# Optimization experiments

Hardware: AMD Instinct MI355X
Metric: run time of the kernel (lower is better)

The kernel has to match this reference:

```python
import jax, jax.numpy as jnp
import numpy as np

B, L, D = 2, 1024, 1024
H, KV, CH = 16, 4, 8          # attn heads, kv heads, context-manager heads
HD = D // H                   # 64
E, K, FF = 8, 2, 4 * D        # experts, top-k, ffn hidden
DC = 4                        # conv kernel size
EPS = 1e-6


def setup_inputs() -> dict:
    key = jax.random.key(0)
    ks = jax.random.split(key, 32)
    s = 0.02
    n = lambda k, shp: jax.random.normal(k, shp, jnp.float32) * s
    return {
        'x': jax.random.normal(ks[0], (B, L, D), jnp.float32),
        'mask': jnp.ones((B, L), jnp.int32),
        'w_rms1': jnp.ones((D,), jnp.float32),
        'w_rms2': jnp.ones((D,), jnp.float32),
        'w_rms3': jnp.ones((D,), jnp.float32),
        'w_rms4': jnp.ones((D,), jnp.float32),
        'Wq': n(ks[1], (D, D)), 'Wk': n(ks[2], (D, KV * HD)),
        'Wv': n(ks[3], (D, KV * HD)), 'Wo': n(ks[4], (D, D)),
        'Cq': n(ks[5], (D, D)), 'Ck': n(ks[6], (D, D)),
        'Cv': n(ks[7], (D, D)), 'Co': n(ks[8], (D, D)),
        'Wi': n(ks[9], (D, 2 * D)), 'bi': jnp.zeros((2 * D,), jnp.float32),
        'conv_w': n(ks[10], (D, 1, DC)), 'conv_b': jnp.zeros((D,), jnp.float32),
        'Wod': n(ks[11], (D, D)), 'bod': jnp.zeros((D,), jnp.float32),
        'w_gate': n(ks[12], (E, D)),
        'W1': n(ks[13], (E, D, FF)), 'b1': jnp.zeros((E, FF), jnp.float32),
        'W2': n(ks[14], (E, FF, D)), 'b2': jnp.zeros((E, D), jnp.float32),
    }


def _rmsnorm(x, w):
    rms = jnp.sqrt(jnp.mean(x * x, axis=-1, keepdims=True) + EPS)
    return w * (x / rms)


def _mha(x, mask, Wq, Wk, Wv, Wo, nh, nkv):
    b, l, d = x.shape
    hd = d // nh
    q = (x @ Wq).reshape(b, l, nh, hd)
    k = (x @ Wk).reshape(b, l, nkv, hd)
    v = (x @ Wv).reshape(b, l, nkv, hd)
    if nh != nkv:
        rep = nh // nkv
        k = jnp.repeat(k, rep, axis=2)
        v = jnp.repeat(v, rep, axis=2)
    scores = jnp.einsum('bqhd,bkhd->bhqk', q, k) * (hd ** -0.5)
    scores = jnp.where(mask[:, None, None, :] == 0, -jnp.inf, scores)
    attn = jax.nn.softmax(scores, axis=-1)
    out = jnp.einsum('bhqk,bkhd->bqhd', attn, v).reshape(b, l, d)
    return out @ Wo


def _deltanet(x, Wi, bi, conv_w, conv_b, Wod, bod):
    gv = x @ Wi + bi
    gate, value = jnp.split(gv, 2, axis=-1)
    # depthwise causal conv1d (kernel DC, left pad DC-1, truncated to L)
    v_ncl = jnp.transpose(value, (0, 2, 1))  # [B, D, L]
    conv = jax.lax.conv_general_dilated(
        v_ncl, conv_w, window_strides=(1,), padding=[(DC - 1, 0)],
        feature_group_count=D, dimension_numbers=('NCH', 'OIH', 'NCH'))
    conv = conv + conv_b[None, :, None]
    conv = jnp.transpose(conv, (0, 2, 1))  # [B, L, D]
    gated = conv * jax.nn.silu(gate)
    return gated @ Wod + bod


def _moe(x, w_gate, W1, b1, W2, b2):
    b, l, d = x.shape
    flat = x.reshape(-1, d)                                  # [T, D]
    gate = jax.nn.softmax(flat @ w_gate.T, axis=-1)          # [T, E]
    topk_scores, topk_idx = jax.lax.top_k(gate, K)           # [T, K]
    onehot = jax.nn.one_hot(topk_idx, E, dtype=flat.dtype)   # [T, K, E]
    combine = jnp.sum(topk_scores[..., None] * onehot, axis=1)  # [T, E]
    h = jnp.einsum('td,edh->teh', flat, W1) + b1
    h = jax.nn.gelu(h, approximate=False)
    y = jnp.einsum('teh,ehd->ted', h, W2) + b2
    out = jnp.einsum('ted,te->td', y, combine)
    return out.reshape(b, l, d)


def reference(x, mask, w_rms1, w_rms2, w_rms3, w_rms4,
              Wq, Wk, Wv, Wo, Cq, Ck, Cv, Co,
              Wi, bi, conv_w, conv_b, Wod, bod,
              w_gate, W1, b1, W2, b2):
    # eval mode: dropout = identity. multi_token_pred output is discarded by the block.
    res1 = x
    h = _rmsnorm(x, w_rms1)
    h = res1 + _mha(h, mask, Wq, Wk, Wv, Wo, H, KV)
    res2 = h
    # ContextManager stand-in: 8-head softmax self-attention (source unavailable)
    cm = _mha(h, mask, Cq, Ck, Cv, Co, CH, CH)
    h = res2 + cm
    res3 = h
    g = _rmsnorm(h, w_rms2)
    h = res3 + _deltanet(g, Wi, bi, conv_w, conv_b, Wod, bod)
    res4 = h
    g = _rmsnorm(h, w_rms3)
    h = res4 + _moe(g, w_gate, W1, b1, W2, b2)
    h = _rmsnorm(h, w_rms4)
    return h
```

## Files before the change

kernel.cpp:

```cpp
#include <hip/hip_runtime.h>
#include <hip/hip_bf16.h>
#include <math.h>

#define T_TOK 2048
#define B_SZ 2
#define L_SEQ 1024
#define D_MOD 1024
#define N_H 16
#define N_KV 4
#define N_CH 8
#define N_E 8
#define FF_DIM 4096
#define DC_K 4
#define EPS_F 1e-6f

typedef unsigned short u16;
typedef unsigned int u32;
typedef short s16x8 __attribute__((ext_vector_type(8)));
typedef u16 u16x8 __attribute__((ext_vector_type(8)));
typedef float f32x4 __attribute__((ext_vector_type(4)));
struct alignas(8) U16x4 { u16 a, b, c, d; };

__device__ __forceinline__ float gelu_exact(float x) {
    return 0.5f * x * (1.0f + erff(x * 0.70710678118654752f));
}
__device__ __forceinline__ u16 f2bf(float f) {
    u32 x = __float_as_uint(f);
    return (u16)((x + 0x7fffu + ((x >> 16) & 1u)) >> 16);
}
__device__ __forceinline__ float b2f(u16 u) {
    return __uint_as_float(((u32)u) << 16);
}
__device__ __forceinline__ void gload_lds16(const u16* g, u16* l) {
    __builtin_amdgcn_global_load_lds(
        (const __attribute__((address_space(1))) u32*)g,
        (__attribute__((address_space(3))) u32*)l, 16, 0, 0);
}

struct TDesc {
    const float* src;
    u16* dst;
    int R, C, dstStride, dstRowOff, tileBase, nPerMat;
};
struct TPack { TDesc d[12]; };

__global__ __launch_bounds__(256) void transpose_all(TPack p) {
    __shared__ float ts[64][65];
    int t = blockIdx.x;
    int i = 0;
#pragma unroll
    for (int j = 1; j < 12; ++j)
        if (t >= p.d[j].tileBase) i = j;
    TDesc d = p.d[i];
    int local = t - d.tileBase;
    int e = local / d.nPerMat;
    local -= e * d.nPerMat;
    int ntx = d.C >> 6;
    int bx = local % ntx, by = local / ntx;
    const float* src = d.src + (size_t)e * d.R * d.C;
    u16* dst = d.dst + (size_t)e * (size_t)d.C * d.dstStride;
    int c0 = bx * 64, r0 = by * 64;
    int tid = threadIdx.x;
#pragma unroll
    for (int k = 0; k < 4; ++k) {
        int fidx = k * 256 + tid;
        int r = fidx >> 4, c4 = (fidx & 15) << 2;
        float4 v = *(const float4*)(src + (size_t)(r0 + r) * d.C + c0 + c4);
        ts[r][c4] = v.x; ts[r][c4 + 1] = v.y; ts[r][c4 + 2] = v.z; ts[r][c4 + 3] = v.w;
    }
    __syncthreads();
#pragma unroll
    for (int k = 0; k < 2; ++k) {
        int idx = k * 256 + tid;
        int c = idx >> 3;
        int r8 = (idx & 7) << 3;
        u16x8 o;
#pragma unroll
        for (int j = 0; j < 8; ++j) o[j] = f2bf(ts[r8 + j][c]);
        *(u16x8*)(dst + (size_t)(d.dstRowOff + c0 + c) * d.dstStride + r0 + r8) = o;
    }
}

__global__ __launch_bounds__(256) void rmsnorm_kernel(const float* __restrict__ x,
                                                      const float* __restrict__ w,
                                                      float* __restrict__ fo,
                                                      u16* __restrict__ bo) {
    int row = blockIdx.x;
    int tid = threadIdx.x;
    const float* xr = x + (size_t)row * D_MOD;
    float4 v = ((const float4*)xr)[tid];
    float ss = v.x * v.x + v.y * v.y + v.z * v.z + v.w * v.w;
    __shared__ float red[256];
    red[tid] = ss;
    __syncthreads();
    for (int s = 128; s > 0; s >>= 1) {
        if (tid < s) red[tid] += red[tid + s];
        __syncthreads();
    }
    float inv = 1.0f / sqrtf(red[0] * (1.0f / D_MOD) + EPS_F);
    float4 wv = ((const float4*)w)[tid];
    float4 o;
    o.x = v.x * inv * wv.x;
    o.y = v.y * inv * wv.y;
    o.z = v.z * inv * wv.z;
    o.w = v.w * inv * wv.w;
    if (fo) ((float4*)(fo + (size_t)row * D_MOD))[tid] = o;
    if (bo) {
        U16x4 b;
        b.a = f2bf(o.x); b.b = f2bf(o.y); b.c = f2bf(o.z); b.d = f2bf(o.w);
        *(U16x4*)(bo + (size_t)row * D_MOD + tid * 4) = b;
    }
}

template <int MODE, int GELU, int OUTF, int OUTB, int BM>
__global__ __launch_bounds__(256) void mfma_gemm(const u16* __restrict__ A,
                                                 const u16* __restrict__ BT,
                                                 const float* __restrict__ bias,
                                                 const float* __restrict__ res,
                                                 float* __restrict__ C,
                                                 u16* __restrict__ Cb,
                                                 const int* __restrict__ list,
                                                 const int* __restrict__ offs,
                                                 const int* __restrict__ counts,
                                                 int M, int N, int K, int nx) {
    constexpr int PWR = BM / 2;
    constexpr int MI = PWR / 16;
    constexpr int NI = 4;
    constexpr int NAI = (BM >= 64) ? (BM / 64) : 1;
    __shared__ u16 ldsA[2][BM * 32];
    __shared__ u16 ldsB[2][128 * 32];
    int tid = threadIdx.x;
    int lane = tid & 63, w = tid >> 6;
    int wr = w >> 1, wc = w & 1;
    int bx, by, e;
    if (MODE == 0) {
        bx = blockIdx.x; by = blockIdx.y; e = 0;
    } else {
        int id = blockIdx.x;
        e = id & 7;
        int r = id >> 3;
        bx = r % nx;
        by = r / nx;
    }
    int cnt, off;
    if (MODE == 0) { cnt = M; off = 0; }
    else { cnt = counts[e]; off = offs[e]; }
    int m0 = by * BM;
    if (m0 >= cnt) return;
    int n0 = bx * 128;
    const u16* Bt = BT + (size_t)e * (size_t)N * K;

    const u16* aSrc[NAI];
    const u16* bSrc[2];
#pragma unroll
    for (int j = 0; j < NAI; ++j) {
        int rowA = (BM >= 64) ? (j * 64 + w * 16 + (lane >> 2))
                              : (w * 16 + (lane >> 2));
        int slot = lane & 3;
        int rl = m0 + ((rowA < BM) ? rowA : (BM - 1));
        if (rl >= cnt) rl = cnt - 1;
        size_t ga;
        if (MODE == 1) ga = (size_t)list[off + rl] * K;
        else if (MODE == 2) ga = (size_t)(off + rl) * K;
        else ga = (size_t)rl * K;
        aSrc[j] = A + ga + ((slot ^ ((rowA >> 1) & 3)) << 3);
    }
#pragma unroll
    for (int j = 0; j < 2; ++j) {
        int rowB = j * 64 + w * 16 + (lane >> 2);
        int slot = lane & 3;
        bSrc[j] = Bt + (size_t)(n0 + rowB) * K + ((slot ^ ((rowB >> 1) & 3)) << 3);
    }

    auto stage = [&](int buf, int k0) {
        if constexpr (BM == 32) {
            if (w < 2) gload_lds16(aSrc[0] + k0, &ldsA[buf][w * 512]);
        } else {
#pragma unroll
            for (int j = 0; j < NAI; ++j)
                gload_lds16(aSrc[j] + k0, &ldsA[buf][(j * 256 + w * 64) * 8]);
        }
#pragma unroll
        for (int j = 0; j < 2; ++j)
            gload_lds16(bSrc[j] + k0, &ldsB[buf][(j * 256 + w * 64) * 8]);
    };

    f32x4 acc[MI][NI] = {};
    int r16 = lane & 15, cr = lane >> 4;

    stage(0, 0);
    __syncthreads();
    int cur = 0;
    for (int k0 = 0; k0 < K; k0 += 32) {
        if (k0 + 32 < K) stage(cur ^ 1, k0 + 32);
        s16x8 af[MI], bfr[NI];
#pragma unroll
        for (int mi = 0; mi < MI; ++mi) {
            int row = wr * PWR + mi * 16 + r16;
            af[mi] = *(const s16x8*)&ldsA[cur][row * 32 + ((cr ^ ((row >> 1) & 3)) << 3)];
        }
#pragma unroll
        for (int ni = 0; ni < NI; ++ni) {
            int row = wc * 64 + ni * 16 + r16;
            bfr[ni] = *(const s16x8*)&ldsB[cur][row * 32 + ((cr ^ ((row >> 1) & 3)) << 3)];
        }
#pragma unroll
        for (int mi = 0; mi < MI; ++mi)
#pragma unroll
            for (int ni = 0; ni < NI; ++ni)
                acc[mi][ni] = __builtin_amdgcn_mfma_f32_16x16x32_bf16(af[mi], bfr[ni],
                                                                      acc[mi][ni], 0, 0, 0);
        __syncthreads();
        cur ^= 1;
    }

    const float* bias_e = bias ? (bias + (MODE ? (size_t)e * N : 0)) : nullptr;
#pragma unroll
    for (int mi = 0; mi < MI; ++mi) {
#pragma unroll
        for (int ni = 0; ni < NI; ++ni) {
            int rloc = wr * PWR + mi * 16 + (lane >> 4) * 4;
            int col = n0 + wc * 64 + ni * 16 + (lane & 15);
#pragma unroll
            for (int jj = 0; jj < 4; ++jj) {
                int rl = m0 + rloc + jj;
                if (rl >= cnt) continue;
                float val = acc[mi][ni][jj];
                if (bias_e) val += bias_e[col];
                if (GELU) val = gelu_exact(val);
                size_t crow = (MODE == 0) ? (size_t)rl : (size_t)(off + rl);
                if (res) val += res[crow * N + col];
                if (OUTF) C[crow * N + col] = val;
                if (OUTB) Cb[crow * N + col] = f2bf(val);
            }
        }
    }
}

template <int HD>
__global__ __launch_bounds__(256) void mfma_attn(const u16* __restrict__ Qb,
                                                 const u16* __restrict__ Kb,
                                                 const u16* __restrict__ Vb,
                                                 u16* __restrict__ O,
                                                 int stride, int ostride,
                                                 int nh, int nkv, float scale) {
    constexpr int KT = 64;
    constexpr int CH = HD / 8;
    constexpr int NF = HD / 32;
    constexpr int ND = HD / 16;
    constexpr int VSTR = 72;
    constexpr int NISS = (64 * CH) / (64 * 4);

    __shared__ u16 Kl[64 * HD];
    __shared__ u16 Vt[HD * VSTR];
    __shared__ u16 Pl[4][16 * 72];

    int tid = threadIdx.x, lane = tid & 63, w = tid >> 6;
    int g = lane >> 4, r16 = lane & 15;
    int q0 = blockIdx.x * 64, h = blockIdx.y, b = blockIdx.z;
    int kvh = h / (nh / nkv);

    const u16* Qp = Qb + (size_t)(b * L_SEQ + q0 + w * 16 + r16) * stride + h * HD + g * 8;
    s16x8 qf[NF];
#pragma unroll
    for (int f = 0; f < NF; ++f) qf[f] = *(const s16x8*)(Qp + f * 32);

    const u16* Kbase = Kb + (size_t)(b * L_SEQ) * stride + (size_t)kvh * HD;
    const u16* Vbase = Vb + (size_t)(b * L_SEQ) * stride + (size_t)kvh * HD;

    int srcOffK[NISS];
#pragma unroll
    for (int i = 0; i < NISS; ++i) {
        int ci = (w * NISS + i) * 64 + lane;
        int row = ci / CH;
        int ch = ci % CH;
        srcOffK[i] = row * stride + ((ch ^ (row & 7)) << 3);
    }

    f32x4 ofr[ND] = {};
    float m_r[4], l_r[4];
#pragma unroll
    for (int r = 0; r < 4; ++r) { m_r[r] = -1e30f; l_r[r] = 0.f; }

    for (int kt = 0; kt < L_SEQ / KT; ++kt) {
        const u16* Ksrc = Kbase + (size_t)(kt * KT) * stride;
        const u16* Vsrc = Vbase + (size_t)(kt * KT) * stride;
        __syncthreads();
#pragma unroll
        for (int i = 0; i < NISS; ++i)
            gload_lds16(Ksrc + srcOffK[i], Kl + (size_t)(w * NISS + i) * 512);
#pragma unroll
        for (int half = 0; half < HD / 64; ++half) {
            int dbase = w * 16 + half * 64;
            u16x8 v0 = *(const u16x8*)(Vsrc + (size_t)lane * stride + dbase);
            u16x8 v1 = *(const u16x8*)(Vsrc + (size_t)lane * stride + dbase + 8);
#pragma unroll
            for (int j = 0; j < 8; ++j) {
                Vt[(dbase + j) * VSTR + lane] = v0[j];
                Vt[(dbase + 8 + j) * VSTR + lane] = v1[j];
            }
        }
        __syncthreads();

        f32x4 s[4];
#pragma unroll
        for (int sub = 0; sub < 4; ++sub) {
            f32x4 acc = {};
#pragma unroll
            for (int f = 0; f < NF; ++f) {
                int row = sub * 16 + r16;
                int chunk = (f * 4 + g) ^ (row & 7);
                s16x8 kf = *(const s16x8*)&Kl[(row * CH + chunk) * 8];
                acc = __builtin_amdgcn_mfma_f32_16x16x32_bf16(qf[f], kf, acc, 0, 0, 0);
            }
            s[sub] = acc;
        }

#pragma unroll
        for (int sub = 0; sub < 4; ++sub)
#pragma unroll
            for (int r = 0; r < 4; ++r) s[sub][r] *= scale;
#pragma unroll
        for (int r = 0; r < 4; ++r) {
            float mx = fmaxf(fmaxf(s[0][r], s[1][r]), fmaxf(s[2][r], s[3][r]));
            mx = fmaxf(mx, __shfl_xor(mx, 1));
            mx = fmaxf(mx, __shfl_xor(mx, 2));
            mx = fmaxf(mx, __shfl_xor(mx, 4));
            mx = fmaxf(mx, __shfl_xor(mx, 8));
            float mo = m_r[r];
            float mn = fmaxf(mo, mx);
            float sc = __expf(mo - mn);
            m_r[r] = mn;
            float sum = 0.f;
#pragma unroll
            for (int sub = 0; sub < 4; ++sub) {
                float e = __expf(s[sub][r] - mn);
                s[sub][r] = e;
                sum += e;
            }
            sum += __shfl_xor(sum, 1);
            sum += __shfl_xor(sum, 2);
            sum += __shfl_xor(sum, 4);
            sum += __shfl_xor(sum, 8);
            l_r[r] = l_r[r] * sc + sum;
#pragma unroll
            for (int dsub = 0; dsub < ND; ++dsub) ofr[dsub][r] *= sc;
        }

        u16* Pw = Pl[w];
#pragma unroll
        for (int sub = 0; sub < 4; ++sub)
#pragma unroll
            for (int r = 0; r < 4; ++r) {
                int q = g * 4 + r;
                int k = sub * 16 + r16;
                Pw[q * 72 + (((k >> 3) ^ (q & 7)) << 3) + (k & 7)] = f2bf(s[sub][r]);
            }
        __syncthreads();

        s16x8 pf[2];
#pragma unroll
        for (int ks = 0; ks < 2; ++ks) {
            int chunk = (ks * 4 + g) ^ (r16 & 7);
            pf[ks] = *(const s16x8*)&Pw[r16 * 72 + chunk * 8];
        }
#pragma unroll
        for (int dsub = 0; dsub < ND; ++dsub)
#pragma unroll
            for (int ks = 0; ks < 2; ++ks) {
                s16x8 vf = *(const s16x8*)&Vt[(dsub * 16 + r16) * VSTR + ks * 32 + g * 8];
                ofr[dsub] = __builtin_amdgcn_mfma_f32_16x16x32_bf16(pf[ks], vf, ofr[dsub], 0, 0, 0);
            }
    }

    float inv[4];
#pragma unroll
    for (int r = 0; r < 4; ++r) inv[r] = 1.0f / l_r[r];
#pragma unroll
    for (int dsub = 0; dsub < ND; ++dsub)
#pragma unroll
        for (int r = 0; r < 4; ++r) {
            int q = q0 + w * 16 + g * 4 + r;
            O[(size_t)(b * L_SEQ + q) * ostride + h * HD + dsub * 16 + r16] =
                f2bf(ofr[dsub][r] * inv[r]);
        }
}

__global__ __launch_bounds__(256) void conv_gate_kernel(const u16* __restrict__ gv,
                                                        const float* __restrict__ cw,
                                                        const float* __restrict__ cb,
                                                        u16* __restrict__ gated) {
    int idx = blockIdx.x * 256 + threadIdx.x;
    if (idx >= T_TOK * D_MOD) return;
    int d = idx & (D_MOD - 1);
    int t = idx >> 10;
    int l = t & (L_SEQ - 1);
    float conv = cb[d];
#pragma unroll
    for (int i = 0; i < DC_K; ++i) {
        int lp = l - (DC_K - 1) + i;
        if (lp >= 0)
            conv += b2f(gv[(size_t)(t - l + lp) * (2 * D_MOD) + D_MOD + d]) * cw[d * DC_K + i];
    }
    float gate = b2f(gv[(size_t)t * (2 * D_MOD) + d]);
    float sig = 1.0f / (1.0f + expf(-gate));
    gated[(size_t)t * D_MOD + d] = f2bf(conv * (gate * sig));
}

__global__ __launch_bounds__(256) void route_kernel(const float* __restrict__ g,
                                                    const float* __restrict__ wg,
                                                    int* __restrict__ tIdx,
                                                    float* __restrict__ tScore,
                                                    int* __restrict__ counts) {
    int t = blockIdx.x, tid = threadIdx.x;
    __shared__ float gs[D_MOD];
    __shared__ float logits[N_E];
    ((float4*)gs)[tid] = ((const float4*)(g + (size_t)t * D_MOD))[tid];
    __syncthreads();
    int e = tid >> 5, lane = tid & 31;
    const float* w = wg + (size_t)e * D_MOD;
    float p = 0.f;
    for (int d = lane; d < D_MOD; d += 32) p += gs[d] * w[d];
    for (int o = 16; o > 0; o >>= 1) p += __shfl_down(p, o, 32);
    if (lane == 0) logits[e] = p;
    __syncthreads();
    if (tid == 0) {
        float mx = logits[0];
        for (int e2 = 1; e2 < N_E; ++e2) mx = fmaxf(mx, logits[e2]);
        float pe[N_E];
        float Z = 0.f;
        for (int e2 = 0; e2 < N_E; ++e2) {
            pe[e2] = expf(logits[e2] - mx);
            Z += pe[e2];
        }
        int i0 = 0;
        float b0 = pe[0];
        for (int e2 = 1; e2 < N_E; ++e2)
            if (pe[e2] > b0) { b0 = pe[e2]; i0 = e2; }
        int i1 = -1;
        float b1 = -1.f;
        for (int e2 = 0; e2 < N_E; ++e2)
            if (e2 != i0 && pe[e2] > b1) { b1 = pe[e2]; i1 = e2; }
        float invZ = 1.0f / Z;
        tIdx[t * 2] = i0;
        tIdx[t * 2 + 1] = i1;
        tScore[t * 2] = b0 * invZ;
        tScore[t * 2 + 1] = b1 * invZ;
        atomicAdd(&counts[i0], 1);
        atomicAdd(&counts[i1], 1);
    }
}

__global__ void prefix_kernel(const int* __restrict__ counts, int* __restrict__ offs,
                              int* __restrict__ cursor) {
    if (threadIdx.x == 0) {
        int acc = 0;
        for (int e = 0; e < N_E; ++e) {
            offs[e] = acc;
            acc += counts[e];
            cursor[e] = 0;
        }
    }
}

__global__ __launch_bounds__(256) void fill_kernel(const int* __restrict__ tIdx,
                                                   const int* __restrict__ offs,
                                                   int* __restrict__ cursor,
                                                   int* __restrict__ list,
                                                   int* __restrict__ pairRow) {
    int t = blockIdx.x * 256 + threadIdx.x;
    if (t >= T_TOK) return;
    for (int kk = 0; kk < 2; ++kk) {
        int e = tIdx[t * 2 + kk];
        int pos = atomicAdd(&cursor[e], 1);
        int slot = offs[e] + pos;
        list[slot] = t;
        pairRow[t * 2 + kk] = slot;
    }
}

__global__ __launch_bounds__(256) void combine_rms_kernel(const u16* __restrict__ ysel,
                                                          const float* __restrict__ tScore,
                                                          const int* __restrict__ pairRow,
                                                          const float* __restrict__ h,
                                                          const float* __restrict__ w,
                                                          float* __restrict__ out) {
    int row = blockIdx.x;
    int tid = threadIdx.x;
    float4 v = ((const float4*)(h + (size_t)row * D_MOD))[tid];
    int r0 = pairRow[row * 2], r1 = pairRow[row * 2 + 1];
    float s0 = tScore[row * 2], s1 = tScore[row * 2 + 1];
    U16x4 y0 = *(const U16x4*)(ysel + (size_t)r0 * D_MOD + tid * 4);
    U16x4 y1 = *(const U16x4*)(ysel + (size_t)r1 * D_MOD + tid * 4);
    v.x += s0 * b2f(y0.a) + s1 * b2f(y1.a);
    v.y += s0 * b2f(y0.b) + s1 * b2f(y1.b);
    v.z += s0 * b2f(y0.c) + s1 * b2f(y1.c);
    v.w += s0 * b2f(y0.d) + s1 * b2f(y1.d);
    __shared__ float red[256];
    red[tid] = v.x * v.x + v.y * v.y + v.z * v.z + v.w * v.w;
    __syncthreads();
    for (int s = 128; s > 0; s >>= 1) {
        if (tid < s) red[tid] += red[tid + s];
        __syncthreads();
    }
    float inv = 1.0f / sqrtf(red[0] * (1.0f / D_MOD) + EPS_F);
    float4 wv = ((const float4*)w)[tid];
    float4 o;
    o.x = v.x * inv * wv.x;
    o.y = v.y * inv * wv.y;
    o.z = v.z * inv * wv.z;
    o.w = v.w * inv * wv.w;
    ((float4*)(out + (size_t)row * D_MOD))[tid] = o;
}

extern "C" void kernel_launch(void* const* d_in, const int* in_sizes, int n_in,
                              void* d_out, int out_size, void* d_ws, size_t ws_size,
                              hipStream_t stream) {
    const float* x = (const float*)d_in[0];
    const float* w_rms1 = (const float*)d_in[2];
    const float* w_rms2 = (const float*)d_in[3];
    const float* w_rms3 = (const float*)d_in[4];
    const float* w_rms4 = (const float*)d_in[5];
    const float* Wq = (const float*)d_in[6];
    const float* Wk = (const float*)d_in[7];
    const float* Wv = (const float*)d_in[8];
    const float* Wo = (const float*)d_in[9];
    const float* Cq = (const float*)d_in[10];
    const float* Ck = (const float*)d_in[11];
    const float* Cv = (const float*)d_in[12];
    const float* Co = (const float*)d_in[13];
    const float* Wi = (const float*)d_in[14];
    const float* bi = (const float*)d_in[15];
    const float* conv_w = (const float*)d_in[16];
    const float* conv_b = (const float*)d_in[17];
    const float* Wod = (const float*)d_in[18];
    const float* bod = (const float*)d_in[19];
    const float* w_gate = (const float*)d_in[20];
    const float* W1 = (const float*)d_in[21];
    const float* b1 = (const float*)d_in[22];
    const float* W2 = (const float*)d_in[23];
    const float* b2 = (const float*)d_in[24];
    float* out = (float*)d_out;

    char* ws = (char*)d_ws;
    size_t off = 0;
    auto alloc_f = [&](size_t n) { float* p = (float*)(ws + off); off += n * 4; return p; };
    auto alloc_b = [&](size_t n) { u16* p = (u16*)(ws + off); off += n * 2; return p; };

    u16* qkvT = alloc_b((size_t)1536 * 1024);
    u16* cqkvT = alloc_b((size_t)3072 * 1024);
    u16* WoT = alloc_b((size_t)1024 * 1024);
    u16* CoT = alloc_b((size_t)1024 * 1024);
    u16* WiT = alloc_b((size_t)2048 * 1024);
    u16* WodT = alloc_b((size_t)1024 * 1024);
    u16* W1T = alloc_b((size_t)N_E * FF_DIM * 1024);
    u16* W2T = alloc_b((size_t)N_E * 1024 * FF_DIM);
    const size_t TD = (size_t)T_TOK * D_MOD;
    float* h = alloc_f(TD);
    float* nrm = alloc_f(TD);
    u16* nrm_bf = alloc_b(TD);
    u16* h_bf = alloc_b(TD);
    u16* ab_bf = alloc_b(TD);
    u16* qkv_bf = alloc_b((size_t)T_TOK * 3072);
    u16* gv_bf = alloc_b((size_t)T_TOK * 2048);
    u16* hsel = alloc_b((size_t)2 * T_TOK * FF_DIM);
    u16* ysel = alloc_b((size_t)2 * T_TOK * D_MOD);
    int* counts = (int*)(ws + off); off += N_E * 4;
    int* offs = (int*)(ws + off); off += N_E * 4;
    int* cursor = (int*)(ws + off); off += N_E * 4;
    int* tIdx = (int*)(ws + off); off += 2 * T_TOK * 4;
    int* list = (int*)(ws + off); off += 2 * T_TOK * 4;
    int* pairRow = (int*)(ws + off); off += 2 * T_TOK * 4;
    float* tScore = alloc_f(2 * T_TOK);

    TPack tp;
    int tb = 0;
    auto mkd = [&](int i, const float* s, u16* d, int R, int C, int ds, int ro, int nmat) {
        int per = (C >> 6) * (R >> 6);
        tp.d[i] = TDesc{s, d, R, C, ds, ro, tb, per};
        tb += per * nmat;
    };
    mkd(0, Wq, qkvT, 1024, 1024, 1024, 0, 1);
    mkd(1, Wk, qkvT, 1024, 256, 1024, 1024, 1);
    mkd(2, Wv, qkvT, 1024, 256, 1024, 1280, 1);
    mkd(3, Cq, cqkvT, 1024, 1024, 1024, 0, 1);
    mkd(4, Ck, cqkvT, 1024, 1024, 1024, 1024, 1);
    mkd(5, Cv, cqkvT, 1024, 1024, 1024, 2048, 1);
    mkd(6, Wo, WoT, 1024, 1024, 1024, 0, 1);
    mkd(7, Co, CoT, 1024, 1024, 1024, 0, 1);
    mkd(8, Wi, WiT, 1024, 2048, 1024, 0, 1);
    mkd(9, Wod, WodT, 1024, 1024, 1024, 0, 1);
    mkd(10, W1, W1T, 1024, FF_DIM, 1024, 0, N_E);
    mkd(11, W2, W2T, FF_DIM, 1024, FF_DIM, 0, N_E);
    transpose_all<<<tb, 256, 0, stream>>>(tp);

    rmsnorm_kernel<<<T_TOK, 256, 0, stream>>>(x, w_rms1, nullptr, nrm_bf);
    mfma_gemm<0, 0, 0, 1, 32><<<dim3(12, 64, 1), 256, 0, stream>>>(
        nrm_bf, qkvT, nullptr, nullptr, nullptr, qkv_bf, nullptr, nullptr, nullptr,
        T_TOK, 1536, 1024, 0);
    mfma_attn<64><<<dim3(16, N_H, B_SZ), 256, 0, stream>>>(
        qkv_bf, qkv_bf + 1024, qkv_bf + 1280, ab_bf, 1536, 1024, N_H, N_KV, 0.125f);
    mfma_gemm<0, 0, 1, 1, 32><<<dim3(8, 64, 1), 256, 0, stream>>>(
        ab_bf, WoT, nullptr, x, h, h_bf, nullptr, nullptr, nullptr, T_TOK, 1024, 1024, 0);

    mfma_gemm<0, 0, 0, 1, 32><<<dim3(24, 64, 1), 256, 0, stream>>>(
        h_bf, cqkvT, nullptr, nullptr, nullptr, qkv_bf, nullptr, nullptr, nullptr,
        T_TOK, 3072, 1024, 0);
    mfma_attn<128><<<dim3(16, N_CH, B_SZ), 256, 0, stream>>>(
        qkv_bf, qkv_bf + 1024, qkv_bf + 2048, ab_bf, 3072, 1024, N_CH, N_CH,
        0.088388347648318447f);
    mfma_gemm<0, 0, 1, 0, 32><<<dim3(8, 64, 1), 256, 0, stream>>>(
        ab_bf, CoT, nullptr, h, h, nullptr, nullptr, nullptr, nullptr, T_TOK, 1024, 1024, 0);

    rmsnorm_kernel<<<T_TOK, 256, 0, stream>>>(h, w_rms2, nullptr, nrm_bf);
    mfma_gemm<0, 0, 0, 1, 32><<<dim3(16, 64, 1), 256, 0, stream>>>(
        nrm_bf, WiT, bi, nullptr, nullptr, gv_bf, nullptr, nullptr, nullptr, T_TOK, 2048, 1024, 0);
    conv_gate_kernel<<<(T_TOK * D_MOD) / 256, 256, 0, stream>>>(gv_bf, conv_w, conv_b, ab_bf);
    mfma_gemm<0, 0, 1, 0, 32><<<dim3(8, 64, 1), 256, 0, stream>>>(
        ab_bf, WodT, bod, h, h, nullptr, nullptr, nullptr, nullptr, T_TOK, 1024, 1024, 0);

    rmsnorm_kernel<<<T_TOK, 256, 0, stream>>>(h, w_rms3, nrm, nrm_bf);
    hipMemsetAsync(counts, 0, N_E * sizeof(int), stream);
    route_kernel<<<T_TOK, 256, 0, stream>>>(nrm, w_gate, tIdx, tScore, counts);
    prefix_kernel<<<1, 64, 0, stream>>>(counts, offs, cursor);
    fill_kernel<<<(T_TOK + 255) / 256, 256, 0, stream>>>(tIdx, offs, cursor, list, pairRow);
    mfma_gemm<1, 1, 0, 1, 128><<<32 * 16 * 8, 256, 0, stream>>>(
        nrm_bf, W1T, b1, nullptr, nullptr, hsel, list, offs, counts, T_TOK, FF_DIM, 1024, 32);
    mfma_gemm<2, 0, 0, 1, 32><<<8 * 64 * 8, 256, 0, stream>>>(
        hsel, W2T, b2, nullptr, nullptr, ysel, list, offs, counts, T_TOK, 1024, FF_DIM, 8);
    combine_rms_kernel<<<T_TOK, 256, 0, stream>>>(ysel, tScore, pairRow, h, w_rms4, out);
}
```

Before: 640.0 us.

## Persistent prefetching transpose, attention MFMA priority hints, vectorized conv gate

The weight transpose kernel becomes a grid-stride persistent kernel with 2048 blocks. It prefetches the next tile's loads into registers while the current tile is written out. The attention kernel wraps its MFMA sections in s_setprio to raise wave priority during matrix math. The conv-gate kernel processes 8 channels per thread using 16-byte bf16 vector loads and stores instead of scalar accesses.

New measurement: 650.6 us. No clear change (+1.7%).

```diff
diff --git a/kernel.cpp b/kernel.cpp
--- a/kernel.cpp
+++ b/kernel.cpp
@@ -44,40 +44,63 @@
 };
 struct TPack { TDesc d[12]; };
 
-__global__ __launch_bounds__(256) void transpose_all(TPack p) {
+__global__ __launch_bounds__(256) void transpose_all(TPack p, int nTiles) {
     __shared__ float ts[64][65];
+    int tid = threadIdx.x;
     int t = blockIdx.x;
-    int i = 0;
-#pragma unroll
-    for (int j = 1; j < 12; ++j)
-        if (t >= p.d[j].tileBase) i = j;
-    TDesc d = p.d[i];
-    int local = t - d.tileBase;
-    int e = local / d.nPerMat;
-    local -= e * d.nPerMat;
-    int ntx = d.C >> 6;
-    int bx = local % ntx, by = local / ntx;
-    const float* src = d.src + (size_t)e * d.R * d.C;
-    u16* dst = d.dst + (size_t)e * (size_t)d.C * d.dstStride;
-    int c0 = bx * 64, r0 = by * 64;
-    int tid = threadIdx.x;
-#pragma unroll
-    for (int k = 0; k < 4; ++k) {
-        int fidx = k * 256 + tid;
-        int r = fidx >> 4, c4 = (fidx & 15) << 2;
-        float4 v = *(const float4*)(src + (size_t)(r0 + r) * d.C + c0 + c4);
-        ts[r][c4] = v.x; ts[r][c4 + 1] = v.y; ts[r][c4 + 2] = v.z; ts[r][c4 + 3] = v.w;
-    }
-    __syncthreads();
-#pragma unroll
-    for (int k = 0; k < 2; ++k) {
-        int idx = k * 256 + tid;
-        int c = idx >> 3;
-        int r8 = (idx & 7) << 3;
-        u16x8 o;
-#pragma unroll
-        for (int j = 0; j < 8; ++j) o[j] = f2bf(ts[r8 + j][c]);
-        *(u16x8*)(dst + (size_t)(d.dstRowOff + c0 + c) * d.dstStride + r0 + r8) = o;
+    float4 rg[4];
+    u16* dstB = nullptr;
+    int dstStr = 0;
+
+    auto prep = [&](int tt) {
+        int i = 0;
+#pragma unroll
+        for (int j = 1; j < 12; ++j)
+            if (tt >= p.d[j].tileBase) i = j;
+        TDesc d = p.d[i];
+        int local = tt - d.tileBase;
+        int e = local / d.nPerMat;
+        local -= e * d.nPerMat;
+        int ntx = d.C >> 6;
+        int bx = local % ntx, by = local / ntx;
+        const float* src = d.src + (size_t)e * d.R * d.C + (size_t)(by * 64) * d.C + bx * 64;
+#pragma unroll
+        for (int k = 0; k < 4; ++k) {
+            int fidx = k * 256 + tid;
+            int r = fidx >> 4, c4 = (fidx & 15) << 2;
+            rg[k] = *(const float4*)(src + (size_t)r * d.C + c4);
+        }
+        dstB = d.dst + (size_t)e * d.C * d.dstStride +
+               (size_t)(d.dstRowOff + bx * 64) * d.dstStride + by * 64;
+        dstStr = d.dstStride;
+    };
+
+    if (t < nTiles) prep(t);
+    for (; t < nTiles; t += gridDim.x) {
+#pragma unroll
+        for (int k = 0; k < 4; ++k) {
+            int fidx = k * 256 + tid;
+            int r = fidx >> 4, c4 = (fidx & 15) << 2;
+            ts[r][c4] = rg[k].x;
+            ts[r][c4 + 1] = rg[k].y;
+            ts[r][c4 + 2] = rg[k].z;
+            ts[r][c4 + 3] = rg[k].w;
+        }
+        u16* db = dstB;
+        int dstr = dstStr;
+        __syncthreads();
+        int tn = t + gridDim.x;
+        if (tn < nTiles) prep(tn);
+#pragma unroll
+        for (int k = 0; k < 2; ++k) {
+            int idx = k * 256 + tid;
+            int c = idx >> 3, r8 = (idx & 7) << 3;
+            u16x8 o;
+#pragma unroll
+            for (int j = 0; j < 8; ++j) o[j] = f2bf(ts[r8 + j][c]);
+            *(u16x8*)(db + (size_t)c * dstr + r8) = o;
+        }
+        __syncthreads();
     }
 }
 
@@ -303,6 +326,7 @@
         __syncthreads();
 
         f32x4 s[4];
+        __builtin_amdgcn_s_setprio(1);
 #pragma unroll
         for (int sub = 0; sub < 4; ++sub) {
             f32x4 acc = {};
@@ -315,6 +339,7 @@
             }
             s[sub] = acc;
         }
+        __builtin_amdgcn_s_setprio(0);
 
 #pragma unroll
         for (int sub = 0; sub < 4; ++sub)
@@ -364,6 +389,7 @@
             int chunk = (ks * 4 + g) ^ (r16 & 7);
             pf[ks] = *(const s16x8*)&Pw[r16 * 72 + chunk * 8];
         }
+        __builtin_amdgcn_s_setprio(1);
 #pragma unroll
         for (int dsub = 0; dsub < ND; ++dsub)
 #pragma unroll
@@ -371,6 +397,7 @@
                 s16x8 vf = *(const s16x8*)&Vt[(dsub * 16 + r16) * VSTR + ks * 32 + g * 8];
                 ofr[dsub] = __builtin_amdgcn_mfma_f32_16x16x32_bf16(pf[ks], vf, ofr[dsub], 0, 0, 0);
             }
+        __builtin_amdgcn_s_setprio(0);
     }
 
     float inv[4];
@@ -391,20 +418,31 @@
                                                         const float* __restrict__ cb,
                                                         u16* __restrict__ gated) {
     int idx = blockIdx.x * 256 + threadIdx.x;
-    if (idx >= T_TOK * D_MOD) return;
-    int d = idx & (D_MOD - 1);
-    int t = idx >> 10;
+    if (idx >= T_TOK * D_MOD / 8) return;
+    int d8 = (idx & 127) << 3;
+    int t = idx >> 7;
     int l = t & (L_SEQ - 1);
-    float conv = cb[d];
+    float conv[8];
+#pragma unroll
+    for (int j = 0; j < 8; ++j) conv[j] = cb[d8 + j];
 #pragma unroll
     for (int i = 0; i < DC_K; ++i) {
         int lp = l - (DC_K - 1) + i;
-        if (lp >= 0)
-            conv += b2f(gv[(size_t)(t - l + lp) * (2 * D_MOD) + D_MOD + d]) * cw[d * DC_K + i];
-    }
-    float gate = b2f(gv[(size_t)t * (2 * D_MOD) + d]);
-    float sig = 1.0f / (1.0f + expf(-gate));
-    gated[(size_t)t * D_MOD + d] = f2bf(conv * (gate * sig));
+        if (lp >= 0) {
+            u16x8 v8 = *(const u16x8*)(gv + (size_t)(t - l + lp) * (2 * D_MOD) + D_MOD + d8);
+#pragma unroll
+            for (int j = 0; j < 8; ++j) conv[j] += b2f(v8[j]) * cw[(d8 + j) * DC_K + i];
+        }
+    }
+    u16x8 g8 = *(const u16x8*)(gv + (size_t)t * (2 * D_MOD) + d8);
+    u16x8 o;
+#pragma unroll
+    for (int j = 0; j < 8; ++j) {
+        float gate = b2f(g8[j]);
+        float sig = 1.0f / (1.0f + expf(-gate));
+        o[j] = f2bf(conv[j] * (gate * sig));
+    }
+    *(u16x8*)(gated + (size_t)t * D_MOD + d8) = o;
 }
 
 __global__ __launch_bounds__(256) void route_kernel(const float* __restrict__ g,
@@ -592,7 +630,7 @@
     mkd(9, Wod, WodT, 1024, 1024, 1024, 0, 1);
     mkd(10, W1, W1T, 1024, FF_DIM, 1024, 0, N_E);
     mkd(11, W2, W2T, FF_DIM, 1024, FF_DIM, 0, N_E);
-    transpose_all<<<tb, 256, 0, stream>>>(tp);
+    transpose_all<<<2048, 256, 0, stream>>>(tp, tb);
 
     rmsnorm_kernel<<<T_TOK, 256, 0, stream>>>(x, w_rms1, nullptr, nrm_bf);
     mfma_gemm<0, 0, 0, 1, 32><<<dim3(12, 64, 1), 256, 0, stream>>>(
@@ -615,7 +653,7 @@
     rmsnorm_kernel<<<T_TOK, 256, 0, stream>>>(h, w_rms2, nullptr, nrm_bf);
     mfma_gemm<0, 0, 0, 1, 32><<<dim3(16, 64, 1), 256, 0, stream>>>(
         nrm_bf, WiT, bi, nullptr, nullptr, gv_bf, nullptr, nullptr, nullptr, T_TOK, 2048, 1024, 0);
-    conv_gate_kernel<<<(T_TOK * D_MOD) / 256, 256, 0, stream>>>(gv_bf, conv_w, conv_b, ab_bf);
+    conv_gate_kernel<<<(T_TOK * D_MOD / 8 + 255) / 256, 256, 0, stream>>>(gv_bf, conv_w, conv_b, ab_bf);
     mfma_gemm<0, 0, 1, 0, 32><<<dim3(8, 64, 1), 256, 0, stream>>>(
         ab_bf, WodT, bod, h, h, nullptr, nullptr, nullptr, nullptr, T_TOK, 1024, 1024, 0);
 
```
